# Kernel tuning notes

Hardware: AMD Instinct MI355X
Metric: run time of the kernel (lower is better)

The kernel has to match this reference:

```python
import jax, jax.numpy as jnp
import numpy as np

NUM_USERS = 200000
NUM_ITEMS = 100000
EMBED_DIM = 64
N_LAYERS = 3
NNZ = 6000000
BATCH = 16384
N_NODES = NUM_USERS + NUM_ITEMS


def setup_inputs() -> dict:
    key = jax.random.key(0)
    k1, k2, k3, k4, k5, k6, k7 = jax.random.split(key, 7)
    user_emb = 0.01 * jax.random.normal(k1, (NUM_USERS, EMBED_DIM), dtype=jnp.float32)
    item_emb = 0.01 * jax.random.normal(k2, (NUM_ITEMS, EMBED_DIM), dtype=jnp.float32)
    adj_rows = jax.random.randint(k3, (NNZ,), 0, N_NODES, dtype=jnp.int32)
    adj_cols = jax.random.randint(k4, (NNZ,), 0, N_NODES, dtype=jnp.int32)
    # positive normalized-adjacency-like values (roughly 1/deg scale)
    adj_vals = jax.random.uniform(k5, (NNZ,), dtype=jnp.float32) * 0.1
    user_ids = jax.random.randint(k6, (BATCH,), 0, NUM_USERS, dtype=jnp.int32)
    item_ids = jax.random.randint(k7, (BATCH,), 0, NUM_ITEMS, dtype=jnp.int32)
    return {
        "user_emb": user_emb,
        "item_emb": item_emb,
        "adj_rows": adj_rows,
        "adj_cols": adj_cols,
        "adj_vals": adj_vals,
        "user_ids": user_ids,
        "item_ids": item_ids,
    }


def reference(user_emb, item_emb, adj_rows, adj_cols, adj_vals, user_ids, item_ids):
    # propagate: repeated SpMM over adjacency with running accumulation
    all_emb = jnp.concatenate([user_emb, item_emb], axis=0)  # [N, D]
    acc = all_emb  # running sum of layer embeddings (fuses stack+mean)
    x = all_emb
    for _ in range(N_LAYERS):
        # SpMM: x_new[r] = sum_e adj_vals[e] * x[adj_cols[e]] for rows r
        msgs = adj_vals[:, None] * x[adj_cols]  # [nnz, D]
        x = jax.ops.segment_sum(msgs, adj_rows, num_segments=N_NODES)
        acc = acc + x
    mean_emb = acc / jnp.float32(N_LAYERS + 1)  # mean over layer outputs
    user_embs = mean_emb[:NUM_USERS]
    item_embs = mean_emb[NUM_USERS:]
    u = user_embs[user_ids]  # [B, D]
    i = item_embs[item_ids]  # [B, D]
    scores = jnp.sum(u * i, axis=1)  # [B]
    return scores
```

## Files before the change

kernel.cpp:

```cpp
#include <hip/hip_runtime.h>

#define EMBED_DIM 64
#define NBLK_A 256
#define BUCKET_SHIFT 9
#define BUCKET_ROWS 512
#define MAX_NBUCK 640
#define SCAN2_CHUNK 2048
#define COL_BITS 19

typedef float fx4 __attribute__((ext_vector_type(4)));
typedef _Float16 h8v __attribute__((ext_vector_type(8)));

__global__ void convert_x_kernel(const float* __restrict__ ue, const float* __restrict__ ie,
                                 _Float16* __restrict__ xh, int nu_elems, int total) {
    int i = blockIdx.x * blockDim.x + threadIdx.x;
    int stride = gridDim.x * blockDim.x;
    int n8 = total >> 3;
    int nu8 = nu_elems >> 3;
    for (; i < n8; i += stride) {
        const float4* src = (i < nu8) ? (const float4*)(ue) + 2 * i
                                      : (const float4*)(ie) + 2 * (i - nu8);
        float4 lo = src[0];
        float4 hi = src[1];
        h8v o;
        o[0] = (_Float16)lo.x; o[1] = (_Float16)lo.y;
        o[2] = (_Float16)lo.z; o[3] = (_Float16)lo.w;
        o[4] = (_Float16)hi.x; o[5] = (_Float16)hi.y;
        o[6] = (_Float16)hi.z; o[7] = (_Float16)hi.w;
        reinterpret_cast<h8v*>(xh)[i] = o;
    }
}

__global__ __launch_bounds__(256) void bucket_count_kernel(
    const int* __restrict__ rows, int* __restrict__ blockCounts,
    int nnz, int nbuck, int chunk) {
    __shared__ int hist[MAX_NBUCK];
    int t = threadIdx.x, blk = blockIdx.x;
    for (int i = t; i < nbuck; i += 256) hist[i] = 0;
    __syncthreads();
    int e0 = blk * chunk;
    int e1 = min(e0 + chunk, nnz);
    for (int e = e0 + t * 4; e < e1; e += 1024) {
        int4 r4 = *reinterpret_cast<const int4*>(rows + e);
        atomicAdd(&hist[r4.x >> BUCKET_SHIFT], 1);
        atomicAdd(&hist[r4.y >> BUCKET_SHIFT], 1);
        atomicAdd(&hist[r4.z >> BUCKET_SHIFT], 1);
        atomicAdd(&hist[r4.w >> BUCKET_SHIFT], 1);
    }
    __syncthreads();
    for (int u = t; u < nbuck; u += 256)
        blockCounts[u * NBLK_A + blk] = hist[u];
}

__global__ void scan8_phase1(const int* __restrict__ in, int* __restrict__ bsum, int n) {
    __shared__ int wsum[4];
    int t = threadIdx.x, b = blockIdx.x;
    int i0 = b * SCAN2_CHUNK + t * 8;
    int s = 0;
    #pragma unroll
    for (int k = 0; k < 8; ++k) { int i = i0 + k; if (i < n) s += in[i]; }
    #pragma unroll
    for (int off = 1; off < 64; off <<= 1) s += __shfl_xor(s, off);
    if ((t & 63) == 0) wsum[t >> 6] = s;
    __syncthreads();
    if (t == 0) bsum[b] = wsum[0] + wsum[1] + wsum[2] + wsum[3];
}

__global__ void scan_phase2(const int* __restrict__ bsum, int* __restrict__ boff, int nb) {
    __shared__ int lds[512];
    int t = threadIdx.x;
    lds[t] = (t < nb) ? bsum[t] : 0;
    __syncthreads();
    for (int off = 1; off < 512; off <<= 1) {
        int v = (t >= off) ? lds[t - off] : 0;
        __syncthreads();
        lds[t] += v;
        __syncthreads();
    }
    if (t < nb) boff[t] = (t == 0) ? 0 : lds[t - 1];
}

__global__ void scan8_phase3(const int* __restrict__ in, const int* __restrict__ boff,
                             int* __restrict__ out, int n) {
    __shared__ int wexcl[4];
    int t = threadIdx.x, b = blockIdx.x;
    int lane = t & 63, w = t >> 6;
    int i0 = b * SCAN2_CHUNK + t * 8;
    int c[8];
    int s = 0;
    #pragma unroll
    for (int k = 0; k < 8; ++k) { int i = i0 + k; c[k] = (i < n) ? in[i] : 0; s += c[k]; }
    int incl = s;
    #pragma unroll
    for (int off = 1; off < 64; off <<= 1) {
        int u = __shfl_up(incl, off);
        if (lane >= off) incl += u;
    }
    if (lane == 63) wexcl[w] = incl;
    __syncthreads();
    int wbase = 0;
    for (int ww = 0; ww < w; ++ww) wbase += wexcl[ww];
    int run = incl - s + wbase + boff[b];
    #pragma unroll
    for (int k = 0; k < 8; ++k) {
        int i = i0 + k;
        if (i < n) { out[i] = run; run += c[k]; }
    }
}

__global__ __launch_bounds__(256) void bucket_scatter_kernel(
    const int* __restrict__ rows, const int* __restrict__ cols,
    const float* __restrict__ vals, const int* __restrict__ scanOut,
    int2* __restrict__ smeta, int nnz, int nbuck, int chunk) {
    __shared__ int cur[MAX_NBUCK];
    int t = threadIdx.x, blk = blockIdx.x;
    for (int u = t; u < nbuck; u += 256) cur[u] = scanOut[u * NBLK_A + blk];
    __syncthreads();
    int e0 = blk * chunk;
    int e1 = min(e0 + chunk, nnz);
    for (int e = e0 + t * 4; e < e1; e += 1024) {
        int4   r4 = *reinterpret_cast<const int4*>(rows + e);
        int4   c4 = *reinterpret_cast<const int4*>(cols + e);
        float4 v4 = *reinterpret_cast<const float4*>(vals + e);
        int p0 = atomicAdd(&cur[r4.x >> BUCKET_SHIFT], 1);
        smeta[p0] = make_int2(((r4.x & (BUCKET_ROWS - 1)) << COL_BITS) | c4.x, __float_as_int(v4.x));
        int p1 = atomicAdd(&cur[r4.y >> BUCKET_SHIFT], 1);
        smeta[p1] = make_int2(((r4.y & (BUCKET_ROWS - 1)) << COL_BITS) | c4.y, __float_as_int(v4.y));
        int p2 = atomicAdd(&cur[r4.z >> BUCKET_SHIFT], 1);
        smeta[p2] = make_int2(((r4.z & (BUCKET_ROWS - 1)) << COL_BITS) | c4.z, __float_as_int(v4.z));
        int p3 = atomicAdd(&cur[r4.w >> BUCKET_SHIFT], 1);
        smeta[p3] = make_int2(((r4.w & (BUCKET_ROWS - 1)) << COL_BITS) | c4.w, __float_as_int(v4.w));
    }
}

__global__ __launch_bounds__(256) void bucket_build_kernel(
    const int2* __restrict__ smeta, const int* __restrict__ scanOut,
    int2* __restrict__ perm, int* __restrict__ row_ptr,
    int nnz, int n_nodes, int nbuck) {
    __shared__ int hist[BUCKET_ROWS], excl[BUCKET_ROWS], cur[BUCKET_ROWS];
    __shared__ int wex[4];
    int t = threadIdx.x, b = blockIdx.x;
    int lane = t & 63, w = t >> 6;
    int ebeg = scanOut[b * NBLK_A];
    int eend = (b + 1 < nbuck) ? scanOut[(b + 1) * NBLK_A] : nnz;
    hist[t] = 0; hist[t + 256] = 0;
    __syncthreads();
    for (int e = ebeg + t; e < eend; e += 256)
        atomicAdd(&hist[smeta[e].x >> COL_BITS], 1);
    __syncthreads();
    int a = hist[2 * t], bcnt = hist[2 * t + 1];
    int s = a + bcnt;
    int incl = s;
    #pragma unroll
    for (int off = 1; off < 64; off <<= 1) {
        int u = __shfl_up(incl, off);
        if (lane >= off) incl += u;
    }
    if (lane == 63) wex[w] = incl;
    __syncthreads();
    int wbase = 0;
    for (int ww = 0; ww < w; ++ww) wbase += wex[ww];
    int es = wbase + incl - s;
    excl[2 * t] = es;
    excl[2 * t + 1] = es + a;
    cur[2 * t] = es;
    cur[2 * t + 1] = es + a;
    __syncthreads();
    int base_row = b << BUCKET_SHIFT;
    for (int r = t; r < BUCKET_ROWS; r += 256) {
        int gr = base_row + r;
        if (gr < n_nodes) row_ptr[gr] = ebeg + excl[r];
    }
    if (b == 0 && t == 0) row_ptr[n_nodes] = nnz;
    for (int e = ebeg + t; e < eend; e += 256) {
        int2 m = smeta[e];
        int l = m.x >> COL_BITS;
        int p = atomicAdd(&cur[l], 1);
        perm[ebeg + p] = make_int2(m.x & ((1 << COL_BITS) - 1), m.y);
    }
}

__global__ void init_bacc_kernel(const float* __restrict__ ue, const float* __restrict__ ie,
                                 const int* __restrict__ uids, const int* __restrict__ iids,
                                 float* __restrict__ uacc, float* __restrict__ iacc, int batch) {
    int t = blockIdx.x * blockDim.x + threadIdx.x;
    if (t >= batch * 16) return;
    int b = t >> 4;
    int q = t & 15;
    const float4* ue4 = (const float4*)ue;
    const float4* ie4 = (const float4*)ie;
    ((float4*)uacc)[t] = ue4[(long)uids[b] * 16 + q];
    ((float4*)iacc)[t] = ie4[(long)iids[b] * 16 + q];
}

__global__ __launch_bounds__(256) void spmm_csr_h_kernel(
    const int* __restrict__ row_ptr, const int2* __restrict__ perm,
    const _Float16* __restrict__ x, _Float16* __restrict__ y, int n_nodes) {
    int lane = threadIdx.x & 63;
    int row = (blockIdx.x * blockDim.x + threadIdx.x) >> 6;
    if (row >= n_nodes) return;
    int start = row_ptr[row];
    int end   = row_ptr[row + 1];
    int sub  = lane >> 3;
    int dimq = lane & 7;
    const h8v* x8 = reinterpret_cast<const h8v*>(x);
    float acc0[8], acc1[8];
    #pragma unroll
    for (int k = 0; k < 8; ++k) { acc0[k] = 0.f; acc1[k] = 0.f; }
    for (int base = start; base < end; base += 16) {
        int e0 = base + sub;
        int e1 = e0 + 8;
        int2 p0 = (e0 < end) ? perm[e0] : make_int2(0, 0);
        int2 p1 = (e1 < end) ? perm[e1] : make_int2(0, 0);
        float v0 = __int_as_float(p0.y);
        float v1 = __int_as_float(p1.y);
        h8v xv0 = x8[(long)p0.x * 8 + dimq];
        h8v xv1 = x8[(long)p1.x * 8 + dimq];
        #pragma unroll
        for (int k = 0; k < 8; ++k) acc0[k] = fmaf(v0, (float)xv0[k], acc0[k]);
        #pragma unroll
        for (int k = 0; k < 8; ++k) acc1[k] = fmaf(v1, (float)xv1[k], acc1[k]);
    }
    float accf[8];
    #pragma unroll
    for (int k = 0; k < 8; ++k) accf[k] = acc0[k] + acc1[k];
    #pragma unroll
    for (int off = 8; off < 64; off <<= 1) {
        #pragma unroll
        for (int k = 0; k < 8; ++k) accf[k] += __shfl_xor(accf[k], off);
    }
    if (sub == 0) {
        h8v o;
        #pragma unroll
        for (int k = 0; k < 8; ++k) o[k] = (_Float16)accf[k];
        reinterpret_cast<h8v*>(y)[(long)row * 8 + dimq] = o;
    }
}

__global__ __launch_bounds__(256) void spmm_batch_h_kernel(
    const int* __restrict__ row_ptr, const int2* __restrict__ perm,
    const _Float16* __restrict__ x,
    const int* __restrict__ uids, const int* __restrict__ iids,
    float* __restrict__ uacc, float* __restrict__ iacc,
    int batch, int num_users) {
    int lane = threadIdx.x & 63;
    int w = (blockIdx.x * blockDim.x + threadIdx.x) >> 6;
    if (w >= 2 * batch) return;
    int row;
    float* target;
    if (w < batch) { row = uids[w];                     target = uacc + (long)w * EMBED_DIM; }
    else           { row = num_users + iids[w - batch]; target = iacc + (long)(w - batch) * EMBED_DIM; }
    int start = row_ptr[row];
    int end   = row_ptr[row + 1];
    int sub  = lane >> 3;
    int dimq = lane & 7;
    const h8v* x8 = reinterpret_cast<const h8v*>(x);
    float acc0[8], acc1[8];
    #pragma unroll
    for (int k = 0; k < 8; ++k) { acc0[k] = 0.f; acc1[k] = 0.f; }
    for (int base = start; base < end; base += 16) {
        int e0 = base + sub;
        int e1 = e0 + 8;
        int2 p0 = (e0 < end) ? perm[e0] : make_int2(0, 0);
        int2 p1 = (e1 < end) ? perm[e1] : make_int2(0, 0);
        float v0 = __int_as_float(p0.y);
        float v1 = __int_as_float(p1.y);
        h8v xv0 = x8[(long)p0.x * 8 + dimq];
        h8v xv1 = x8[(long)p1.x * 8 + dimq];
        #pragma unroll
        for (int k = 0; k < 8; ++k) acc0[k] = fmaf(v0, (float)xv0[k], acc0[k]);
        #pragma unroll
        for (int k = 0; k < 8; ++k) acc1[k] = fmaf(v1, (float)xv1[k], acc1[k]);
    }
    float accf[8];
    #pragma unroll
    for (int k = 0; k < 8; ++k) accf[k] = acc0[k] + acc1[k];
    #pragma unroll
    for (int off = 8; off < 64; off <<= 1) {
        #pragma unroll
        for (int k = 0; k < 8; ++k) accf[k] += __shfl_xor(accf[k], off);
    }
    if (sub == 0) {
        fx4* t4 = reinterpret_cast<fx4*>(target) + dimq * 2;
        fx4 lo = t4[0], hi = t4[1];
        lo.x += accf[0]; lo.y += accf[1]; lo.z += accf[2]; lo.w += accf[3];
        hi.x += accf[4]; hi.y += accf[5]; hi.z += accf[6]; hi.w += accf[7];
        t4[0] = lo; t4[1] = hi;
    }
}

__global__ void bacc_add_h_kernel(const _Float16* __restrict__ y,
                                  const int* __restrict__ uids, const int* __restrict__ iids,
                                  float* __restrict__ uacc, float* __restrict__ iacc,
                                  int batch, int num_users) {
    int t = blockIdx.x * blockDim.x + threadIdx.x;
    if (t >= batch * 8) return;
    int b = t >> 3;
    int q = t & 7;
    const h8v* y8 = (const h8v*)y;
    h8v u = y8[(long)uids[b] * 8 + q];
    h8v v = y8[((long)num_users + iids[b]) * 8 + q];
    float4* ua = (float4*)uacc + (long)b * 16 + q * 2;
    float4* ia = (float4*)iacc + (long)b * 16 + q * 2;
    float4 a0 = ua[0], a1 = ua[1];
    a0.x += (float)u[0]; a0.y += (float)u[1]; a0.z += (float)u[2]; a0.w += (float)u[3];
    a1.x += (float)u[4]; a1.y += (float)u[5]; a1.z += (float)u[6]; a1.w += (float)u[7];
    ua[0] = a0; ua[1] = a1;
    float4 c0 = ia[0], c1 = ia[1];
    c0.x += (float)v[0]; c0.y += (float)v[1]; c0.z += (float)v[2]; c0.w += (float)v[3];
    c1.x += (float)v[4]; c1.y += (float)v[5]; c1.z += (float)v[6]; c1.w += (float)v[7];
    ia[0] = c0; ia[1] = c1;
}

__global__ void score_kernel(const float* __restrict__ uacc, const float* __restrict__ iacc,
                             float* __restrict__ out, int batch) {
    int lane = threadIdx.x & 63;
    int w = (blockIdx.x * blockDim.x + threadIdx.x) >> 6;
    if (w >= batch) return;
    float p = uacc[(long)w * EMBED_DIM + lane] * iacc[(long)w * EMBED_DIM + lane];
    #pragma unroll
    for (int off = 32; off > 0; off >>= 1) p += __shfl_down(p, off);
    if (lane == 0) out[w] = p * (1.0f / 16.0f);
}

extern "C" void kernel_launch(void* const* d_in, const int* in_sizes, int n_in,
                              void* d_out, int out_size, void* d_ws, size_t ws_size,
                              hipStream_t stream) {
    const float* user_emb = (const float*)d_in[0];
    const float* item_emb = (const float*)d_in[1];
    const int*   adj_rows = (const int*)d_in[2];
    const int*   adj_cols = (const int*)d_in[3];
    const float* adj_vals = (const float*)d_in[4];
    const int*   user_ids = (const int*)d_in[5];
    const int*   item_ids = (const int*)d_in[6];
    float* out = (float*)d_out;

    const int num_users = in_sizes[0] / EMBED_DIM;
    const int num_items = in_sizes[1] / EMBED_DIM;
    const int n_nodes   = num_users + num_items;
    const int nnz       = in_sizes[2];
    const int batch     = in_sizes[5];

    const long node_elems = (long)n_nodes * EMBED_DIM;
    const long bacc_elems = (long)batch * EMBED_DIM;

    const int nbuck = (n_nodes + BUCKET_ROWS - 1) >> BUCKET_SHIFT;
    const int nscan = nbuck * NBLK_A;
    const int nscan_blocks = (nscan + SCAN2_CHUNK - 1) / SCAN2_CHUNK;

    char* wp = (char*)d_ws;
    _Float16* xh   = (_Float16*)wp;      wp += node_elems * sizeof(_Float16);
    _Float16* bufA = (_Float16*)wp;      wp += node_elems * sizeof(_Float16);
    _Float16* bufB = (_Float16*)wp;      wp += node_elems * sizeof(_Float16);
    float* uacc = (float*)wp;            wp += bacc_elems * sizeof(float);
    float* iacc = (float*)wp;            wp += bacc_elems * sizeof(float);
    int*   row_ptr = (int*)wp;           wp += (size_t)(n_nodes + 4) * sizeof(int);
    int*   bsum    = (int*)wp;           wp += 512 * sizeof(int);
    int*   boff    = (int*)wp;           wp += 512 * sizeof(int);
    int*   blockCounts = (int*)wp;       wp += (size_t)nscan * sizeof(int);
    int*   scanOut     = (int*)wp;       wp += (size_t)nscan * sizeof(int);
    wp = (char*)(((uintptr_t)wp + 15) & ~(uintptr_t)15);
    int2*  perm    = (int2*)wp;          wp += (size_t)nnz * sizeof(int2);

    int2* smeta = (int2*)bufA;

    const int chunkA = (((nnz + NBLK_A - 1) / NBLK_A) + 1023) & ~1023;

    bucket_count_kernel<<<NBLK_A, 256, 0, stream>>>(adj_rows, blockCounts, nnz, nbuck, chunkA);
    scan8_phase1<<<nscan_blocks, 256, 0, stream>>>(blockCounts, bsum, nscan);
    scan_phase2<<<1, 512, 0, stream>>>(bsum, boff, nscan_blocks);
    scan8_phase3<<<nscan_blocks, 256, 0, stream>>>(blockCounts, boff, scanOut, nscan);
    bucket_scatter_kernel<<<NBLK_A, 256, 0, stream>>>(adj_rows, adj_cols, adj_vals,
                                                      scanOut, smeta, nnz, nbuck, chunkA);
    bucket_build_kernel<<<nbuck, 256, 0, stream>>>(smeta, scanOut, perm,
                                                   row_ptr, nnz, n_nodes, nbuck);

    convert_x_kernel<<<2048, 256, 0, stream>>>(user_emb, item_emb, xh,
                                               num_users * EMBED_DIM, (int)node_elems);

    {
        int blocks = (batch * 16 + 255) / 256;
        init_bacc_kernel<<<blocks, 256, 0, stream>>>(user_emb, item_emb, user_ids, item_ids,
                                                     uacc, iacc, batch);
    }

    const int spmm_blocks = ((n_nodes * 64) + 255) / 256;
    const int bblocks = (batch * 8 + 255) / 256;

    spmm_csr_h_kernel<<<spmm_blocks, 256, 0, stream>>>(row_ptr, perm, xh, bufA, n_nodes);
    bacc_add_h_kernel<<<bblocks, 256, 0, stream>>>(bufA, user_ids, item_ids,
                                                   uacc, iacc, batch, num_users);

    spmm_csr_h_kernel<<<spmm_blocks, 256, 0, stream>>>(row_ptr, perm, bufA, bufB, n_nodes);
    bacc_add_h_kernel<<<bblocks, 256, 0, stream>>>(bufB, user_ids, item_ids,
                                                   uacc, iacc, batch, num_users);

    {
        int waves = 2 * batch;
        int blocks = (waves * 64 + 255) / 256;
        spmm_batch_h_kernel<<<blocks, 256, 0, stream>>>(row_ptr, perm, bufB,
                                                        user_ids, item_ids,
                                                        uacc, iacc, batch, num_users);
    }

    {
        int blocks = (batch * 64 + 255) / 256;
        score_kernel<<<blocks, 256, 0, stream>>>(uacc, iacc, out, batch);
    }
}
```

Measured before the change: 507.8 us.

## Stage bucket permutation in LDS, use nontemporal loads and 32-bit gather addressing

The bucket build kernel now scatters each bucket's entries into a shared-memory staging array, then writes them to the permuted array with coalesced stores, falling back to direct scatter when a bucket exceeds capacity. The edge-list reads in the count and scatter kernels use nontemporal loads so streaming data does not pollute the cache. The SpMM kernels compute gather and store addresses with 32-bit shift-or byte offsets instead of 64-bit index multiplication. The staging buffer uses about 120KB of LDS per block, which cuts build-kernel occupancy to one block per CU.

```diff
diff --git a/kernel.cpp b/kernel.cpp
--- a/kernel.cpp
+++ b/kernel.cpp
@@ -7,8 +7,11 @@
 #define MAX_NBUCK 640
 #define SCAN2_CHUNK 2048
 #define COL_BITS 19
+#define STAGE_CAP 15360
 
 typedef float fx4 __attribute__((ext_vector_type(4)));
+typedef int   ix4 __attribute__((ext_vector_type(4)));
+typedef float fv4 __attribute__((ext_vector_type(4)));
 typedef _Float16 h8v __attribute__((ext_vector_type(8)));
 
 __global__ void convert_x_kernel(const float* __restrict__ ue, const float* __restrict__ ie,
@@ -41,7 +44,7 @@
     int e0 = blk * chunk;
     int e1 = min(e0 + chunk, nnz);
     for (int e = e0 + t * 4; e < e1; e += 1024) {
-        int4 r4 = *reinterpret_cast<const int4*>(rows + e);
+        ix4 r4 = __builtin_nontemporal_load(reinterpret_cast<const ix4*>(rows + e));
         atomicAdd(&hist[r4.x >> BUCKET_SHIFT], 1);
         atomicAdd(&hist[r4.y >> BUCKET_SHIFT], 1);
         atomicAdd(&hist[r4.z >> BUCKET_SHIFT], 1);
@@ -119,9 +122,9 @@
     int e0 = blk * chunk;
     int e1 = min(e0 + chunk, nnz);
     for (int e = e0 + t * 4; e < e1; e += 1024) {
-        int4   r4 = *reinterpret_cast<const int4*>(rows + e);
-        int4   c4 = *reinterpret_cast<const int4*>(cols + e);
-        float4 v4 = *reinterpret_cast<const float4*>(vals + e);
+        ix4 r4 = __builtin_nontemporal_load(reinterpret_cast<const ix4*>(rows + e));
+        ix4 c4 = __builtin_nontemporal_load(reinterpret_cast<const ix4*>(cols + e));
+        fv4 v4 = __builtin_nontemporal_load(reinterpret_cast<const fv4*>(vals + e));
         int p0 = atomicAdd(&cur[r4.x >> BUCKET_SHIFT], 1);
         smeta[p0] = make_int2(((r4.x & (BUCKET_ROWS - 1)) << COL_BITS) | c4.x, __float_as_int(v4.x));
         int p1 = atomicAdd(&cur[r4.y >> BUCKET_SHIFT], 1);
@@ -139,6 +142,7 @@
     int nnz, int n_nodes, int nbuck) {
     __shared__ int hist[BUCKET_ROWS], excl[BUCKET_ROWS], cur[BUCKET_ROWS];
     __shared__ int wex[4];
+    __shared__ int2 stage[STAGE_CAP];
     int t = threadIdx.x, b = blockIdx.x;
     int lane = t & 63, w = t >> 6;
     int ebeg = scanOut[b * NBLK_A];
@@ -172,11 +176,24 @@
         if (gr < n_nodes) row_ptr[gr] = ebeg + excl[r];
     }
     if (b == 0 && t == 0) row_ptr[n_nodes] = nnz;
-    for (int e = ebeg + t; e < eend; e += 256) {
-        int2 m = smeta[e];
-        int l = m.x >> COL_BITS;
-        int p = atomicAdd(&cur[l], 1);
-        perm[ebeg + p] = make_int2(m.x & ((1 << COL_BITS) - 1), m.y);
+    int nbe = eend - ebeg;
+    if (nbe <= STAGE_CAP) {
+        for (int e = ebeg + t; e < eend; e += 256) {
+            int2 m = smeta[e];
+            int l = m.x >> COL_BITS;
+            int p = atomicAdd(&cur[l], 1);
+            stage[p] = make_int2(m.x & ((1 << COL_BITS) - 1), m.y);
+        }
+        __syncthreads();
+        for (int i = t; i < nbe; i += 256)
+            perm[ebeg + i] = stage[i];
+    } else {
+        for (int e = ebeg + t; e < eend; e += 256) {
+            int2 m = smeta[e];
+            int l = m.x >> COL_BITS;
+            int p = atomicAdd(&cur[l], 1);
+            perm[ebeg + p] = make_int2(m.x & ((1 << COL_BITS) - 1), m.y);
+        }
     }
 }
 
@@ -202,8 +219,8 @@
     int start = row_ptr[row];
     int end   = row_ptr[row + 1];
     int sub  = lane >> 3;
-    int dimq = lane & 7;
-    const h8v* x8 = reinterpret_cast<const h8v*>(x);
+    unsigned dimb = ((unsigned)(lane & 7)) << 4;
+    const char* xb = reinterpret_cast<const char*>(x);
     float acc0[8], acc1[8];
     #pragma unroll
     for (int k = 0; k < 8; ++k) { acc0[k] = 0.f; acc1[k] = 0.f; }
@@ -214,8 +231,8 @@
         int2 p1 = (e1 < end) ? perm[e1] : make_int2(0, 0);
         float v0 = __int_as_float(p0.y);
         float v1 = __int_as_float(p1.y);
-        h8v xv0 = x8[(long)p0.x * 8 + dimq];
-        h8v xv1 = x8[(long)p1.x * 8 + dimq];
+        h8v xv0 = *reinterpret_cast<const h8v*>(xb + ((((unsigned)p0.x) << 7) | dimb));
+        h8v xv1 = *reinterpret_cast<const h8v*>(xb + ((((unsigned)p1.x) << 7) | dimb));
         #pragma unroll
         for (int k = 0; k < 8; ++k) acc0[k] = fmaf(v0, (float)xv0[k], acc0[k]);
         #pragma unroll
@@ -233,7 +250,7 @@
         h8v o;
         #pragma unroll
         for (int k = 0; k < 8; ++k) o[k] = (_Float16)accf[k];
-        reinterpret_cast<h8v*>(y)[(long)row * 8 + dimq] = o;
+        *reinterpret_cast<h8v*>(reinterpret_cast<char*>(y) + ((((unsigned)row) << 7) | dimb)) = o;
     }
 }
 
@@ -254,7 +271,8 @@
     int end   = row_ptr[row + 1];
     int sub  = lane >> 3;
     int dimq = lane & 7;
-    const h8v* x8 = reinterpret_cast<const h8v*>(x);
+    unsigned dimb = ((unsigned)dimq) << 4;
+    const char* xb = reinterpret_cast<const char*>(x);
     float acc0[8], acc1[8];
     #pragma unroll
     for (int k = 0; k < 8; ++k) { acc0[k] = 0.f; acc1[k] = 0.f; }
@@ -265,8 +283,8 @@
         int2 p1 = (e1 < end) ? perm[e1] : make_int2(0, 0);
         float v0 = __int_as_float(p0.y);
         float v1 = __int_as_float(p1.y);
-        h8v xv0 = x8[(long)p0.x * 8 + dimq];
-        h8v xv1 = x8[(long)p1.x * 8 + dimq];
+        h8v xv0 = *reinterpret_cast<const h8v*>(xb + ((((unsigned)p0.x) << 7) | dimb));
+        h8v xv1 = *reinterpret_cast<const h8v*>(xb + ((((unsigned)p1.x) << 7) | dimb));
         #pragma unroll
         for (int k = 0; k < 8; ++k) acc0[k] = fmaf(v0, (float)xv0[k], acc0[k]);
         #pragma unroll
```

Measured after the change: 497.4 us. 1.02x faster.
